# Performance work log

Measured on AMD Instinct MI355X. Metric: run time of the kernel, lower is better.

The kernel has to match this reference:

```python
import jax, jax.numpy as jnp
import numpy as np

R = 7        # rcnn_crop_size[cls_ind]
SCALE = 4    # cfg['stride']


def _pool1d(x, c0, c1, K):
    # Adaptive max pool along leading axis of x ([F, ...] -> [R, ...]).
    # torch AdaptiveMaxPool bins: start_i = floor(i*L/R), end_i = ceil((i+1)*L/R)
    F = x.shape[0]
    L = c1 - c0
    i = jnp.arange(R)
    starts = c0 + (i * L) // R
    ends = c0 + ((i + 1) * L + R - 1) // R
    idx = starts[:, None] + jnp.arange(K)[None, :]           # [R, K], K bounds max bin length
    g = x[jnp.clip(idx, 0, F - 1)]                           # [R, K, ...]
    valid = (idx < ends[:, None]).reshape((R, K) + (1,) * (x.ndim - 1))
    return jnp.max(jnp.where(valid, g, jnp.finfo(x.dtype).min), axis=1)


def _crop_pool(f, dims_max, p, Ks):
    # One proposal: variable-size crop from f[b] + adaptive max pool to [C,R,R,R].
    b = p[0].astype(jnp.int32)
    center, side = p[2:5], p[5:8]
    c0 = jnp.floor((center - side / 2) / SCALE).astype(jnp.int32)
    c1 = jnp.ceil((center + side / 2) / SCALE).astype(jnp.int32)
    c0 = jnp.maximum(c0, 0)
    c1 = jnp.minimum(c1, dims_max)
    x = f[b]                                                 # [C, Fd, Fh, Fw]
    for ax in range(3):                                      # separable adaptive max pool
        x = jnp.moveaxis(x, ax + 1, 0)
        x = _pool1d(x, c0[ax], c1[ax], Ks[ax])
        x = jnp.moveaxis(x, 0, ax + 1)
    return x                                                 # [C, R, R, R]


def setup_inputs() -> dict:
    key = jax.random.key(0)
    kf, kb, ks, kc, kd = jax.random.split(key, 5)
    B, C, Fs = 4, 64, 32
    N = 96
    f = jax.random.normal(kf, (B, C, Fs, Fs, Fs), dtype=jnp.float32)
    inputs = jnp.zeros((B, 1, 128, 128, 128), dtype=jnp.float32)
    bidx = jax.random.randint(kb, (N, 1), 0, B).astype(jnp.float32)
    score = jax.random.uniform(ks, (N, 1), dtype=jnp.float32)
    centers = jax.random.uniform(kc, (N, 3), minval=24.0, maxval=104.0, dtype=jnp.float32)
    sides = jax.random.uniform(kd, (N, 3), minval=8.0, maxval=48.0, dtype=jnp.float32)
    proposals = jnp.concatenate([bidx, score, centers, sides], axis=1)  # [N, 8]
    return {"f": f, "inputs": inputs, "proposals": proposals, "cls_ind": 0}


def reference(f, inputs, proposals, cls_ind):
    D, H, W = inputs.shape[2], inputs.shape[3], inputs.shape[4]
    dims_max = jnp.array([D // SCALE, H // SCALE, W // SCALE], dtype=jnp.int32)
    # max bin length per axis for any crop length L <= F: ceil(F/R)+1
    Ks = tuple(-(-f.shape[ax + 2] // R) + 1 for ax in range(3))
    return jax.vmap(lambda p: _crop_pool(f, dims_max, p, Ks))(proposals)  # [N, C, R, R, R]
```

## Files before the change

### kernel.cpp

```cpp
#include <hip/hip_runtime.h>
#include <float.h>


#define NTHREADS 384
#define MAXL 14
#define MAXV (MAXL * MAXL * MAXL)

__global__ __launch_bounds__(NTHREADS) void crop_roi_lds(
        const float* __restrict__ f,
        const float* __restrict__ props,
        float* __restrict__ out,
        int C) {
    __shared__ float s[2 * MAXV];
    const int cbase = blockIdx.x * 2;
    const int n = blockIdx.y;
    const int tid = threadIdx.x;

    const float* p = props + (size_t)n * 8;
    const int b = (int)p[0];

    int d0 = (int)floorf((p[2] - p[5] * 0.5f) * 0.25f);
    int d1 = (int)ceilf ((p[2] + p[5] * 0.5f) * 0.25f);
    int h0 = (int)floorf((p[3] - p[6] * 0.5f) * 0.25f);
    int h1 = (int)ceilf ((p[3] + p[6] * 0.5f) * 0.25f);
    int w0 = (int)floorf((p[4] - p[7] * 0.5f) * 0.25f);
    int w1 = (int)ceilf ((p[4] + p[7] * 0.5f) * 0.25f);
    d0 = max(d0, 0); d1 = min(d1, 32);
    h0 = max(h0, 0); h1 = min(h1, 32);
    w0 = max(w0, 0); w1 = min(w1, 32);
    const int Ld = d1 - d0, Lh = h1 - h0, Lw = w1 - w0;

    const float* base0 = f + (((size_t)b * C + cbase) << 15);
    const int nch = min(2, C - cbase);

    if (Ld <= MAXL && Lh <= MAXL && Lw <= MAXL) {
        const int D1 = Lh * Lw;
        const int V  = Ld * D1;
        const unsigned Mdh = (D1 > 1) ? (unsigned)(0x100000000ULL / (unsigned)D1) + 1u : 0u;
        const unsigned Mw  = (Lw > 1) ? (unsigned)(0x100000000ULL / (unsigned)Lw) + 1u : 0u;

        for (int cs = 0; cs < nch; ++cs) {
            const float* basec = base0 + ((size_t)cs << 15);
            float* sc = s + cs * MAXV;
            for (int e = tid; e < V; e += NTHREADS) {
                unsigned d = (D1 > 1) ? __umulhi((unsigned)e, Mdh) : (unsigned)e;
                unsigned r = (unsigned)e - d * (unsigned)D1;
                unsigned h = (Lw > 1) ? __umulhi(r, Mw) : r;
                unsigned w = r - h * (unsigned)Lw;
                sc[e] = basec[(((d0 + (int)d) << 5) + (h0 + (int)h) << 5) + w0 + (int)w];
            }
        }
        __syncthreads();

        for (int t = tid; t < 343 * nch; t += NTHREADS) {
            const int cs = (t >= 343);
            const int o  = t - (cs ? 343 : 0);
            const int i = o / 49;
            const int j = (o / 7) % 7;
            const int k = o % 7;
            const int a0 = (i * Ld) / 7,  a1 = ((i + 1) * Ld + 6) / 7;
            const int b0 = (j * Lh) / 7,  b1 = ((j + 1) * Lh + 6) / 7;
            const int g0 = (k * Lw) / 7,  g1 = ((k + 1) * Lw + 6) / 7;
            float m = -FLT_MAX;
            const float* sc = s + cs * MAXV;
            for (int d = a0; d < a1; ++d) {
                for (int h = b0; h < b1; ++h) {
                    const float* row = sc + (d * Lh + h) * Lw;
                    for (int w = g0; w < g1; ++w) m = fmaxf(m, row[w]);
                }
            }
            out[((size_t)n * C + cbase + cs) * 343 + o] = m;
        }
    } else {
        for (int t = tid; t < 343 * nch; t += NTHREADS) {
            const int cs = (t >= 343);
            const int o  = t - (cs ? 343 : 0);
            const int i = o / 49, j = (o / 7) % 7, k = o % 7;
            const int ds = d0 + (i * Ld) / 7, de = d0 + ((i + 1) * Ld + 6) / 7;
            const int hs = h0 + (j * Lh) / 7, he = h0 + ((j + 1) * Lh + 6) / 7;
            const int ws = w0 + (k * Lw) / 7, we = w0 + ((k + 1) * Lw + 6) / 7;
            float m = -FLT_MAX;
            const float* basec = base0 + ((size_t)cs << 15);
            for (int d = ds; d < de; ++d) {
                for (int h = hs; h < he; ++h) {
                    const float* row = basec + (d << 10) + (h << 5);
                    for (int w = ws; w < we; ++w) m = fmaxf(m, row[w]);
                }
            }
            out[((size_t)n * C + cbase + cs) * 343 + o] = m;
        }
    }
}

extern "C" void kernel_launch(void* const* d_in, const int* in_sizes, int n_in,
                              void* d_out, int out_size, void* d_ws, size_t ws_size,
                              hipStream_t stream) {
    const float* f = (const float*)d_in[0];
    const float* props = (const float*)d_in[2];

    int N = in_sizes[2] / 8;
    int C = out_size / (N * 343);

    dim3 block(NTHREADS);
    dim3 grid((C + 1) / 2, N);
    crop_roi_lds<<<grid, block, 0, stream>>>(f, props, (float*)d_out, C);
}
```

Before: 116.7 us.

## Process four channels per block and share pooling bin math across channels

Each block now handles four channels with 256 threads instead of two channels with 384. In the pooling phase each thread computes one output position and reduces all four channels together, so the bin-boundary arithmetic is done once per position and there are four independent max chains for extra ILP. The shared-memory buffer grows to four crops, which may lower how many blocks fit per CU. The 343 outputs also leave the second pass over 256 threads only partly occupied.

```diff
diff --git a/kernel.cpp b/kernel.cpp
--- a/kernel.cpp
+++ b/kernel.cpp
@@ -2,17 +2,18 @@
 #include <float.h>
 
 
-#define NTHREADS 384
+#define NTHREADS 256
+#define NCH 4
 #define MAXL 14
 #define MAXV (MAXL * MAXL * MAXL)
 
-__global__ __launch_bounds__(NTHREADS) void crop_roi_lds(
+__global__ __launch_bounds__(NTHREADS) void crop_roi_lds4(
         const float* __restrict__ f,
         const float* __restrict__ props,
         float* __restrict__ out,
         int C) {
-    __shared__ float s[2 * MAXV];
-    const int cbase = blockIdx.x * 2;
+    __shared__ float s[NCH * MAXV];
+    const int cbase = blockIdx.x * NCH;
     const int n = blockIdx.y;
     const int tid = threadIdx.x;
 
@@ -31,7 +32,7 @@
     const int Ld = d1 - d0, Lh = h1 - h0, Lw = w1 - w0;
 
     const float* base0 = f + (((size_t)b * C + cbase) << 15);
-    const int nch = min(2, C - cbase);
+    const int nch = min(NCH, C - cbase);
 
     if (Ld <= MAXL && Lh <= MAXL && Lw <= MAXL) {
         const int D1 = Lh * Lw;
@@ -47,47 +48,51 @@
                 unsigned r = (unsigned)e - d * (unsigned)D1;
                 unsigned h = (Lw > 1) ? __umulhi(r, Mw) : r;
                 unsigned w = r - h * (unsigned)Lw;
-                sc[e] = basec[(((d0 + (int)d) << 5) + (h0 + (int)h) << 5) + w0 + (int)w];
+                sc[e] = basec[((((d0 + (int)d) << 5) + (h0 + (int)h)) << 5) + w0 + (int)w];
             }
         }
         __syncthreads();
 
-        for (int t = tid; t < 343 * nch; t += NTHREADS) {
-            const int cs = (t >= 343);
-            const int o  = t - (cs ? 343 : 0);
+        for (int o = tid; o < 343; o += NTHREADS) {
             const int i = o / 49;
             const int j = (o / 7) % 7;
             const int k = o % 7;
             const int a0 = (i * Ld) / 7,  a1 = ((i + 1) * Ld + 6) / 7;
             const int b0 = (j * Lh) / 7,  b1 = ((j + 1) * Lh + 6) / 7;
             const int g0 = (k * Lw) / 7,  g1 = ((k + 1) * Lw + 6) / 7;
-            float m = -FLT_MAX;
-            const float* sc = s + cs * MAXV;
+            float m[NCH];
+#pragma unroll
+            for (int cs = 0; cs < NCH; ++cs) m[cs] = -FLT_MAX;
             for (int d = a0; d < a1; ++d) {
                 for (int h = b0; h < b1; ++h) {
-                    const float* row = sc + (d * Lh + h) * Lw;
-                    for (int w = g0; w < g1; ++w) m = fmaxf(m, row[w]);
+                    const int rowb = (d * Lh + h) * Lw;
+                    for (int w = g0; w < g1; ++w) {
+                        const int idx = rowb + w;
+#pragma unroll
+                        for (int cs = 0; cs < NCH; ++cs)
+                            m[cs] = fmaxf(m[cs], s[cs * MAXV + idx]);
+                    }
                 }
             }
-            out[((size_t)n * C + cbase + cs) * 343 + o] = m;
+            for (int cs = 0; cs < nch; ++cs)
+                out[((size_t)n * C + cbase + cs) * 343 + o] = m[cs];
         }
     } else {
-        for (int t = tid; t < 343 * nch; t += NTHREADS) {
-            const int cs = (t >= 343);
-            const int o  = t - (cs ? 343 : 0);
+        for (int o = tid; o < 343; o += NTHREADS) {
             const int i = o / 49, j = (o / 7) % 7, k = o % 7;
             const int ds = d0 + (i * Ld) / 7, de = d0 + ((i + 1) * Ld + 6) / 7;
             const int hs = h0 + (j * Lh) / 7, he = h0 + ((j + 1) * Lh + 6) / 7;
             const int ws = w0 + (k * Lw) / 7, we = w0 + ((k + 1) * Lw + 6) / 7;
-            float m = -FLT_MAX;
-            const float* basec = base0 + ((size_t)cs << 15);
-            for (int d = ds; d < de; ++d) {
-                for (int h = hs; h < he; ++h) {
-                    const float* row = basec + (d << 10) + (h << 5);
-                    for (int w = ws; w < we; ++w) m = fmaxf(m, row[w]);
-                }
+            for (int cs = 0; cs < nch; ++cs) {
+                float m = -FLT_MAX;
+                const float* basec = base0 + ((size_t)cs << 15);
+                for (int d = ds; d < de; ++d)
+                    for (int h = hs; h < he; ++h) {
+                        const float* row = basec + (d << 10) + (h << 5);
+                        for (int w = ws; w < we; ++w) m = fmaxf(m, row[w]);
+                    }
+                out[((size_t)n * C + cbase + cs) * 343 + o] = m;
             }
-            out[((size_t)n * C + cbase + cs) * 343 + o] = m;
         }
     }
 }
@@ -102,6 +107,6 @@
     int C = out_size / (N * 343);
 
     dim3 block(NTHREADS);
-    dim3 grid((C + 1) / 2, N);
-    crop_roi_lds<<<grid, block, 0, stream>>>(f, props, (float*)d_out, C);
+    dim3 grid((C + NCH - 1) / NCH, N);
+    crop_roi_lds4<<<grid, block, 0, stream>>>(f, props, (float*)d_out, C);
 }
```

Result: faster. 113.4 us (-2.9%).
